# Kernel tuning notes

Hardware: AMD Instinct MI355X
Metric: run time of the kernel (lower is better)

Reference implementation:

```python
import jax, jax.numpy as jnp
import numpy as np

B, N, M, L = 16, 4096, 64, 16
NUM_FREQ, MAX_FREQ = 32, 10.0
WIDTH, NUM_MOD = 256, 512
K_GRAPH, K_INTERP = 8, 3

BANDS = 2.0 ** jnp.linspace(0.0, MAX_FREQ, NUM_FREQ)  # [32]


def setup_inputs() -> dict:
    key = jax.random.key(0)
    ks = jax.random.split(key, 12)
    return {
        "pos_g": jax.random.uniform(ks[0], (B, N, 2), dtype=jnp.float32),
        "pos_z": jax.random.uniform(ks[1], (B, M, 2), dtype=jnp.float32),
        "feat_z": jax.random.normal(ks[2], (B, M, L), dtype=jnp.float32),
        "Wl": jax.random.normal(ks[3], (L, NUM_MOD), dtype=jnp.float32) * 0.25,
        "bl": jnp.zeros((NUM_MOD,), jnp.float32),
        "Wr": jax.random.normal(ks[4], (L, NUM_MOD), dtype=jnp.float32) * 0.25,
        "W0": jax.random.normal(ks[5], (2 * 2 * NUM_FREQ, WIDTH), dtype=jnp.float32) * 0.09,
        "b0": jnp.zeros((WIDTH,), jnp.float32),
        "W1": jax.random.normal(ks[6], (WIDTH, WIDTH), dtype=jnp.float32) * 0.06,
        "b1": jnp.zeros((WIDTH,), jnp.float32),
        "W2": jax.random.normal(ks[7], (WIDTH, 1), dtype=jnp.float32) * 0.06,
        "b2": jnp.zeros((1,), jnp.float32),
    }


def _sqdist(a, b):
    # a: [B,P,2], b: [B,Q,2] -> [B,P,Q]
    return (jnp.sum(a * a, -1)[..., :, None]
            + jnp.sum(b * b, -1)[..., None, :]
            - 2.0 * jnp.einsum('bpd,bqd->bpq', a, b))


_gather = jax.vmap(lambda f, i: f[i])  # f:[M,C], i:[P,K] -> [P,K,C]


def reference(pos_g, pos_z, feat_z, Wl, bl, Wr, W0, b0, W1, b1, W2, b2):
    # --- knn_graph(z.pos, k=8, loop=False) + SAGEConv(mean aggr) ---
    d2_zz = _sqdist(pos_z, pos_z) + 1e10 * jnp.eye(M, dtype=pos_z.dtype)  # mask self-loops
    _, nbr_idx = jax.lax.top_k(-d2_zz, K_GRAPH)                 # [B,M,8]
    neigh = _gather(feat_z, nbr_idx)                            # [B,M,8,L]
    aggr = jnp.mean(neigh, axis=2)                              # [B,M,L]
    features = aggr @ Wl + bl + feat_z @ Wr                     # [B,M,512] (lin_r has no bias)

    # --- knn_interpolate(features, z.pos -> graph.pos, k=3) ---
    d2_gz = _sqdist(pos_g, pos_z)                               # [B,N,M]
    neg_d2, knn_idx = jax.lax.top_k(-d2_gz, K_INTERP)           # [B,N,3]
    w = 1.0 / jnp.maximum(-neg_d2, 1e-16)                       # inverse squared distance
    fk = _gather(features, knn_idx)                             # [B,N,3,512]
    feats_interp = jnp.sum(fk * w[..., None], axis=2) / jnp.sum(w, axis=2, keepdims=True)

    # --- positional embedding (log-sampled bands, no input concat) ---
    winded = (pos_g[:, :, None, :] * BANDS[None, None, :, None]).reshape(B, N, 2 * NUM_FREQ)
    position = jnp.concatenate([jnp.sin(winded), jnp.cos(winded)], axis=-1)  # [B,N,128]

    # --- film_translate: shift-only FiLM through hidden layers ---
    s0 = feats_interp[..., :WIDTH]
    s1 = feats_interp[..., WIDTH:]
    h = jax.nn.relu(position @ W0 + b0 + s0)                    # [B,N,256]
    h = jax.nn.relu(h @ W1 + b1 + s1)                           # [B,N,256]
    out = h @ W2 + b2                                           # [B,N,1]
    return out
```

## Files before the change

kernel.cpp:

```cpp
#include <hip/hip_runtime.h>
#include <cmath>

#define B_ 16
#define N_ 4096
#define M_ 64
#define L_ 16
#define NFREQ 32
#define NMOD 512
#define WIDTH_ 256
#define TIE_EPS 3e-7f


__global__ void __launch_bounds__(256)
feat_kernel(const float* __restrict__ pos_z, const float* __restrict__ feat_z,
            const float* __restrict__ Wl, const float* __restrict__ bl,
            const float* __restrict__ Wr, float* __restrict__ feats) {
  const int b  = blockIdx.x >> 3;
  const int cs = (blockIdx.x & 7) * 64;
  const int t  = threadIdx.x;
  __shared__ float zx[M_], zy[M_];
  __shared__ float fz[M_][L_];
  __shared__ float ag[M_][L_];
  if (t < M_) { zx[t] = pos_z[(b*M_+t)*2+0]; zy[t] = pos_z[(b*M_+t)*2+1]; }
  for (int i = t; i < M_*L_; i += 256) fz[i>>4][i&15] = feat_z[b*M_*L_ + i];
  __syncthreads();
  if (t < M_) {
    float bd[9]; int bi[9];
#pragma unroll
    for (int q=0;q<9;q++){ bd[q]=1e30f; bi[q]=0; }
    const float px = zx[t], py = zy[t];
    const float st = __fadd_rn(__fmul_rn(px,px), __fmul_rn(py,py));
    for (int j=0;j<M_;j++){
      if (j==t) continue;
      const float sj  = __fadd_rn(__fmul_rn(zx[j],zx[j]), __fmul_rn(zy[j],zy[j]));
      const float dot = __fmaf_rn(py, zy[j], __fmul_rn(px, zx[j]));
      const float d   = __fmaf_rn(-2.f, dot, __fadd_rn(st, sj));
      if (d < bd[8]) {
        int q = 8;
        while (q > 0 && bd[q-1] > d) { bd[q]=bd[q-1]; bi[q]=bi[q-1]; --q; }
        bd[q]=d; bi[q]=j;
      }
    }
    const bool hedge = (bd[8] - bd[7]) < TIE_EPS;
#pragma unroll
    for (int l=0;l<L_;l++){
      float s = 0.f;
#pragma unroll
      for (int q=0;q<7;q++) s += fz[bi[q]][l];
      s += hedge ? 0.5f*(fz[bi[7]][l] + fz[bi[8]][l]) : fz[bi[7]][l];
      ag[t][l] = s * 0.125f;
    }
  }
  __syncthreads();
  for (int idx = t; idx < M_*64; idx += 256) {
    const int i = idx >> 6, c = cs + (idx & 63);
    float a = 0.f, r = 0.f;
#pragma unroll
    for (int l=0;l<L_;l++){ a += ag[i][l]*Wl[l*NMOD+c]; r += fz[i][l]*Wr[l*NMOD+c]; }
    feats[b*M_*NMOD + i*NMOD + c] = (a + bl[c]) + r;
  }
}

__global__ void __launch_bounds__(256, 3)
fused_kernel(const float* __restrict__ pos_g, const float* __restrict__ pos_z,
             const float* __restrict__ feats,
             const float* __restrict__ W0, const float* __restrict__ b0,
             const float* __restrict__ W1, const float* __restrict__ b1,
             const float* __restrict__ W2, const float* __restrict__ b2,
             float* __restrict__ out) {
  const int b    = blockIdx.x >> 7;
  const int tile = blockIdx.x & 127;
  const int t    = threadIdx.x;
  const int g0   = tile * 32;

  __shared__ float zx[64], zy[64], gx[32], gy[32];
  __shared__ float band[NFREQ];
  __shared__ float wn[32][4];
  __shared__ int   wi[32][4];
  __shared__ float pe[32*132];
  __shared__ float h0[32*260];

  if (t < 64)      { zx[t]=pos_z[(b*64+t)*2]; zy[t]=pos_z[(b*64+t)*2+1]; }
  else if (t < 96) { const int p=t-64;
                     gx[p]=pos_g[((size_t)b*N_+g0+p)*2];
                     gy[p]=pos_g[((size_t)b*N_+g0+p)*2+1]; }
  else if (t < 96+NFREQ) { const int f=t-96;
                     const float step = __fdiv_rn(10.f, 31.f);
                     band[f] = (f==NFREQ-1) ? 1024.f
                                            : exp2f(__fmul_rn((float)f, step)); }
  __syncthreads();

  if (t < 32) {
    const float px = gx[t], py = gy[t];
    const float sg = __fadd_rn(__fmul_rn(px,px), __fmul_rn(py,py));
    float d0=1e30f,d1=1e30f,d2v=1e30f,d3=1e30f; int i0=0,i1=0,i2=0,i3=0;
    for (int j=0;j<64;j++){
      const float sz  = __fadd_rn(__fmul_rn(zx[j],zx[j]), __fmul_rn(zy[j],zy[j]));
      const float dot = __fmaf_rn(py, zy[j], __fmul_rn(px, zx[j]));
      const float d   = __fmaf_rn(-2.f, dot, __fadd_rn(sg, sz));
      if (d < d3){
        if (d < d2v){
          if (d < d1){
            if (d < d0){ d3=d2v;i3=i2; d2v=d1;i2=i1; d1=d0;i1=i0; d0=d;i0=j; }
            else       { d3=d2v;i3=i2; d2v=d1;i2=i1; d1=d;  i1=j; }
          } else       { d3=d2v;i3=i2; d2v=d;  i2=j; }
        } else         { d3=d;  i3=j; }
      }
    }
    const float wA0 = __fdiv_rn(1.f, fmaxf(d0, 1e-16f));
    const float wA1 = __fdiv_rn(1.f, fmaxf(d1, 1e-16f));
    const float wA2 = __fdiv_rn(1.f, fmaxf(d2v,1e-16f));
    const float invA = __fdiv_rn(1.f, __fadd_rn(__fadd_rn(wA0,wA1),wA2));
    if ((d3 - d2v) < TIE_EPS) {
      const float wB3 = __fdiv_rn(1.f, fmaxf(d3, 1e-16f));
      const float invB = __fdiv_rn(1.f, __fadd_rn(__fadd_rn(wA0,wA1),wB3));
      wn[t][0] = 0.5f*(wA0*invA + wA0*invB);
      wn[t][1] = 0.5f*(wA1*invA + wA1*invB);
      wn[t][2] = 0.5f*wA2*invA;
      wn[t][3] = 0.5f*wB3*invB;
    } else {
      wn[t][0] = __fmul_rn(wA0,invA);
      wn[t][1] = __fmul_rn(wA1,invA);
      wn[t][2] = __fmul_rn(wA2,invA);
      wn[t][3] = 0.f;
    }
    wi[t][0]=i0; wi[t][1]=i1; wi[t][2]=i2; wi[t][3]=i3;
  }

  for (int idx=t; idx<32*128; idx+=256){
    const int p = idx >> 7, k = idx & 127;
    const int kk = k & 63;
    const float arg = ((kk & 1) ? gy[p] : gx[p]) * band[kk>>1];
    pe[p*132+k] = (k < 64) ? sinf(arg) : cosf(arg);
  }
  __syncthreads();

  const int tp = t >> 4, tc = t & 15;
  const int p0 = tp*2;

  for (int cb=0; cb<4; ++cb){
    const int c0 = cb*64 + tc*4;
    float acc[2][4];
    {
      const float4 b4 = *reinterpret_cast<const float4*>(&b0[c0]);
      const float* bb = reinterpret_cast<const float*>(&b4);
#pragma unroll
      for (int i=0;i<2;i++){
        const int p = p0+i;
        float s[4] = {0.f,0.f,0.f,0.f};
#pragma unroll
        for (int q=0;q<4;q++){
          const float wq = wn[p][q];
          const float4 f4 = *reinterpret_cast<const float4*>(
              &feats[((size_t)(b*64 + wi[p][q]))*NMOD + c0]);
          const float* ff = reinterpret_cast<const float*>(&f4);
#pragma unroll
          for (int j=0;j<4;j++) s[j] += wq*ff[j];
        }
#pragma unroll
        for (int j=0;j<4;j++) acc[i][j] = bb[j] + s[j];
      }
    }
    float4 wb[4], pb[2];
#pragma unroll
    for (int r=0;r<4;r++) wb[r] = *reinterpret_cast<const float4*>(&W0[(size_t)r*WIDTH_ + c0]);
#pragma unroll
    for (int i=0;i<2;i++) pb[i] = *reinterpret_cast<const float4*>(&pe[(p0+i)*132]);
    for (int k=0;k<128;k+=4){
      float4 wc[4], pc[2];
#pragma unroll
      for (int r=0;r<4;r++) wc[r]=wb[r];
#pragma unroll
      for (int i=0;i<2;i++) pc[i]=pb[i];
      if (k+4 < 128){
#pragma unroll
        for (int r=0;r<4;r++) wb[r] = *reinterpret_cast<const float4*>(&W0[(size_t)(k+4+r)*WIDTH_ + c0]);
#pragma unroll
        for (int i=0;i<2;i++) pb[i] = *reinterpret_cast<const float4*>(&pe[(p0+i)*132 + k+4]);
      }
#pragma unroll
      for (int i=0;i<2;i++){
        const float* pv = reinterpret_cast<const float*>(&pc[i]);
#pragma unroll
        for (int r=0;r<4;r++){
          const float* wr = reinterpret_cast<const float*>(&wc[r]);
#pragma unroll
          for (int j=0;j<4;j++) acc[i][j] += pv[r]*wr[j];
        }
      }
    }
#pragma unroll
    for (int i=0;i<2;i++){
      float4 o; float* ov = reinterpret_cast<float*>(&o);
#pragma unroll
      for (int j=0;j<4;j++) ov[j] = fmaxf(acc[i][j], 0.f);
      *reinterpret_cast<float4*>(&h0[(p0+i)*260 + c0]) = o;
    }
  }
  __syncthreads();

  float op[2] = {0.f,0.f};
  for (int cb=0; cb<4; ++cb){
    const int c0 = cb*64 + tc*4;
    float acc[2][4];
    {
      const float4 b4 = *reinterpret_cast<const float4*>(&b1[c0]);
      const float* bb = reinterpret_cast<const float*>(&b4);
#pragma unroll
      for (int i=0;i<2;i++){
        const int p = p0+i;
        float s[4] = {0.f,0.f,0.f,0.f};
#pragma unroll
        for (int q=0;q<4;q++){
          const float wq = wn[p][q];
          const float4 f4 = *reinterpret_cast<const float4*>(
              &feats[((size_t)(b*64 + wi[p][q]))*NMOD + WIDTH_ + c0]);
          const float* ff = reinterpret_cast<const float*>(&f4);
#pragma unroll
          for (int j=0;j<4;j++) s[j] += wq*ff[j];
        }
#pragma unroll
        for (int j=0;j<4;j++) acc[i][j] = bb[j] + s[j];
      }
    }
    float4 wb[4], pb[2];
#pragma unroll
    for (int r=0;r<4;r++) wb[r] = *reinterpret_cast<const float4*>(&W1[(size_t)r*WIDTH_ + c0]);
#pragma unroll
    for (int i=0;i<2;i++) pb[i] = *reinterpret_cast<const float4*>(&h0[(p0+i)*260]);
    for (int k=0;k<256;k+=4){
      float4 wc[4], pc[2];
#pragma unroll
      for (int r=0;r<4;r++) wc[r]=wb[r];
#pragma unroll
      for (int i=0;i<2;i++) pc[i]=pb[i];
      if (k+4 < 256){
#pragma unroll
        for (int r=0;r<4;r++) wb[r] = *reinterpret_cast<const float4*>(&W1[(size_t)(k+4+r)*WIDTH_ + c0]);
#pragma unroll
        for (int i=0;i<2;i++) pb[i] = *reinterpret_cast<const float4*>(&h0[(p0+i)*260 + k+4]);
      }
#pragma unroll
      for (int i=0;i<2;i++){
        const float* pv = reinterpret_cast<const float*>(&pc[i]);
#pragma unroll
        for (int r=0;r<4;r++){
          const float* wr = reinterpret_cast<const float*>(&wc[r]);
#pragma unroll
          for (int j=0;j<4;j++) acc[i][j] += pv[r]*wr[j];
        }
      }
    }
    const float4 w24 = *reinterpret_cast<const float4*>(&W2[c0]);
    const float* w2v = reinterpret_cast<const float*>(&w24);
#pragma unroll
    for (int i=0;i<2;i++){
#pragma unroll
      for (int j=0;j<4;j++) op[i] += fmaxf(acc[i][j],0.f)*w2v[j];
    }
  }
#pragma unroll
  for (int i=0;i<2;i++){
#pragma unroll
    for (int off=1; off<16; off<<=1) op[i] += __shfl_xor(op[i], off, 64);
  }
  if (tc == 0){
    const float bb2 = b2[0];
#pragma unroll
    for (int i=0;i<2;i++) out[(size_t)b*N_ + g0 + p0 + i] = op[i] + bb2;
  }
}

extern "C" void kernel_launch(void* const* d_in, const int* in_sizes, int n_in,
                              void* d_out, int out_size, void* d_ws, size_t ws_size,
                              hipStream_t stream) {
  const float* pos_g  = (const float*)d_in[0];
  const float* pos_z  = (const float*)d_in[1];
  const float* feat_z = (const float*)d_in[2];
  const float* Wl     = (const float*)d_in[3];
  const float* bl     = (const float*)d_in[4];
  const float* Wr     = (const float*)d_in[5];
  const float* W0     = (const float*)d_in[6];
  const float* b0     = (const float*)d_in[7];
  const float* W1     = (const float*)d_in[8];
  const float* b1     = (const float*)d_in[9];
  const float* W2     = (const float*)d_in[10];
  const float* b2     = (const float*)d_in[11];
  float* feats = (float*)d_ws;

  feat_kernel<<<dim3(B_*8), dim3(256), 0, stream>>>(pos_z, feat_z, Wl, bl, Wr, feats);
  fused_kernel<<<dim3(B_*(N_/32)), dim3(256), 0, stream>>>(
      pos_g, pos_z, feats, W0, b0, W1, b1, W2, b2, (float*)d_out);
}
```

Baseline: 482.2 us.

## Split fused MLP into two register-tiled GEMM kernels with global h1 buffer

Replaces the single fused kernel with two kernels. The first builds the positional embedding and computes layer 0 with a 4x16 register-blocked outer-product GEMM, writing h1 to workspace. The second computes layer 1 plus the final projection with a shuffle reduction, and recomputes the kNN weights in each kernel. The feat kernel is also split across more blocks. The aim is better compute density and occupancy, at the cost of a 64MB h1 round trip through global memory and duplicated kNN work; the old fused path is kept as a fallback when the workspace is too small.

```diff
diff --git a/kernel.cpp b/kernel.cpp
--- a/kernel.cpp
+++ b/kernel.cpp
@@ -15,8 +15,8 @@
 feat_kernel(const float* __restrict__ pos_z, const float* __restrict__ feat_z,
             const float* __restrict__ Wl, const float* __restrict__ bl,
             const float* __restrict__ Wr, float* __restrict__ feats) {
-  const int b  = blockIdx.x >> 3;
-  const int cs = (blockIdx.x & 7) * 64;
+  const int b  = blockIdx.x >> 5;
+  const int cs = (blockIdx.x & 31) * 16;
   const int t  = threadIdx.x;
   __shared__ float zx[M_], zy[M_];
   __shared__ float fz[M_][L_];
@@ -52,8 +52,8 @@
     }
   }
   __syncthreads();
-  for (int idx = t; idx < M_*64; idx += 256) {
-    const int i = idx >> 6, c = cs + (idx & 63);
+  for (int idx = t; idx < M_*16; idx += 256) {
+    const int i = idx >> 4, c = cs + (idx & 15);
     float a = 0.f, r = 0.f;
 #pragma unroll
     for (int l=0;l<L_;l++){ a += ag[i][l]*Wl[l*NMOD+c]; r += fz[i][l]*Wr[l*NMOD+c]; }
@@ -61,36 +61,10 @@
   }
 }
 
-__global__ void __launch_bounds__(256, 3)
-fused_kernel(const float* __restrict__ pos_g, const float* __restrict__ pos_z,
-             const float* __restrict__ feats,
-             const float* __restrict__ W0, const float* __restrict__ b0,
-             const float* __restrict__ W1, const float* __restrict__ b1,
-             const float* __restrict__ W2, const float* __restrict__ b2,
-             float* __restrict__ out) {
-  const int b    = blockIdx.x >> 7;
-  const int tile = blockIdx.x & 127;
-  const int t    = threadIdx.x;
-  const int g0   = tile * 32;
-
-  __shared__ float zx[64], zy[64], gx[32], gy[32];
-  __shared__ float band[NFREQ];
-  __shared__ float wn[32][4];
-  __shared__ int   wi[32][4];
-  __shared__ float pe[32*132];
-  __shared__ float h0[32*260];
-
-  if (t < 64)      { zx[t]=pos_z[(b*64+t)*2]; zy[t]=pos_z[(b*64+t)*2+1]; }
-  else if (t < 96) { const int p=t-64;
-                     gx[p]=pos_g[((size_t)b*N_+g0+p)*2];
-                     gy[p]=pos_g[((size_t)b*N_+g0+p)*2+1]; }
-  else if (t < 96+NFREQ) { const int f=t-96;
-                     const float step = __fdiv_rn(10.f, 31.f);
-                     band[f] = (f==NFREQ-1) ? 1024.f
-                                            : exp2f(__fmul_rn((float)f, step)); }
-  __syncthreads();
-
-  if (t < 32) {
+__device__ __forceinline__ void knn3_hedge(
+    int t, const float* zx, const float* zy, const float* gx, const float* gy,
+    float (*wn)[4], int (*wi)[4]) {
+  if (t < 64) {
     const float px = gx[t], py = gy[t];
     const float sg = __fadd_rn(__fmul_rn(px,px), __fmul_rn(py,py));
     float d0=1e30f,d1=1e30f,d2v=1e30f,d3=1e30f; int i0=0,i1=0,i2=0,i3=0;
@@ -126,6 +100,302 @@
     }
     wi[t][0]=i0; wi[t][1]=i1; wi[t][2]=i2; wi[t][3]=i3;
   }
+}
+
+__global__ void __launch_bounds__(256, 4)
+b1_kernel(const float* __restrict__ pos_g, const float* __restrict__ pos_z,
+          const float* __restrict__ feats,
+          const float* __restrict__ W0, const float* __restrict__ b0,
+          float* __restrict__ h1) {
+  const int b    = blockIdx.x >> 6;
+  const int tile = blockIdx.x & 63;
+  const int t    = threadIdx.x;
+  const int g0   = tile * 64;
+
+  __shared__ float zx[64], zy[64], gx[64], gy[64];
+  __shared__ float band[NFREQ];
+  __shared__ float wn[64][4];
+  __shared__ int   wi[64][4];
+  __shared__ __align__(16) float pe_lds[64][20];
+  __shared__ __align__(16) float w_lds[16*256];
+
+  if (t < 64)       { zx[t]=pos_z[(b*64+t)*2]; zy[t]=pos_z[(b*64+t)*2+1]; }
+  else if (t < 128) { const int p=t-64;
+                      gx[p]=pos_g[((size_t)b*N_+g0+p)*2];
+                      gy[p]=pos_g[((size_t)b*N_+g0+p)*2+1]; }
+  else if (t < 128+NFREQ) { const int f=t-128;
+                      const float step = __fdiv_rn(10.f, 31.f);
+                      band[f] = (f==NFREQ-1) ? 1024.f
+                                             : exp2f(__fmul_rn((float)f, step)); }
+  __syncthreads();
+
+  knn3_hedge(t, zx, zy, gx, gy, wn, wi);
+
+  const int tp = t >> 4, tc = t & 15;
+  const int p0 = tp*4;
+
+  float acc[4][4][4];
+#pragma unroll
+  for (int i=0;i<4;i++)
+#pragma unroll
+    for (int g=0;g<4;g++)
+#pragma unroll
+      for (int j=0;j<4;j++) acc[i][g][j] = 0.f;
+
+  for (int ck = 0; ck < 8; ++ck) {
+    __syncthreads();
+    const int base = ck*16*256;
+#pragma unroll
+    for (int e = 0; e < 4; ++e) {
+      const int dw = e*1024 + t*4;
+      *reinterpret_cast<float4*>(&w_lds[dw]) =
+          *reinterpret_cast<const float4*>(&W0[base + dw]);
+    }
+#pragma unroll
+    for (int e = 0; e < 4; ++e) {
+      const int idx = t + e*256;
+      const int p = idx >> 4, kl = idx & 15;
+      const int k = ck*16 + kl;
+      const int kk = k & 63;
+      const float arg = ((kk & 1) ? gy[p] : gx[p]) * band[kk>>1];
+      pe_lds[p][kl] = (k < 64) ? sinf(arg) : cosf(arg);
+    }
+    __syncthreads();
+#pragma unroll
+    for (int ks = 0; ks < 4; ++ks) {
+      float4 pv[4];
+#pragma unroll
+      for (int i=0;i<4;i++)
+        pv[i] = *reinterpret_cast<const float4*>(&pe_lds[p0+i][ks*4]);
+#pragma unroll
+      for (int k=0;k<4;k++){
+        float4 wv[4];
+#pragma unroll
+        for (int g=0; g<4; g++)
+          wv[g] = *reinterpret_cast<const float4*>(&w_lds[(ks*4+k)*256 + g*64 + tc*4]);
+#pragma unroll
+        for (int i=0;i<4;i++){
+          const float pvk = reinterpret_cast<const float*>(&pv[i])[k];
+#pragma unroll
+          for (int g=0; g<4; g++){
+            const float* wvv = reinterpret_cast<const float*>(&wv[g]);
+#pragma unroll
+            for (int j=0;j<4;j++) acc[i][g][j] += pvk*wvv[j];
+          }
+        }
+      }
+    }
+  }
+
+  const size_t prow = (size_t)b*N_ + g0;
+#pragma unroll
+  for (int g=0; g<4; ++g){
+    const int c0 = g*64 + tc*4;
+    const float4 b4 = *reinterpret_cast<const float4*>(&b0[c0]);
+    const float* bb = reinterpret_cast<const float*>(&b4);
+#pragma unroll
+    for (int i=0;i<4;i++){
+      const int p = p0+i;
+      float s[4] = {0.f,0.f,0.f,0.f};
+#pragma unroll
+      for (int q=0;q<4;q++){
+        const float wq = wn[p][q];
+        const float4 f4 = *reinterpret_cast<const float4*>(
+            &feats[((size_t)(b*64 + wi[p][q]))*NMOD + c0]);
+        const float* ff = reinterpret_cast<const float*>(&f4);
+#pragma unroll
+        for (int j=0;j<4;j++) s[j] += wq*ff[j];
+      }
+      float4 o; float* ov = reinterpret_cast<float*>(&o);
+#pragma unroll
+      for (int j=0;j<4;j++) ov[j] = fmaxf(acc[i][g][j] + (bb[j] + s[j]), 0.f);
+      *reinterpret_cast<float4*>(&h1[(prow + p)*WIDTH_ + c0]) = o;
+    }
+  }
+}
+
+__global__ void __launch_bounds__(256, 4)
+b2_kernel(const float* __restrict__ pos_g, const float* __restrict__ pos_z,
+          const float* __restrict__ feats, const float* __restrict__ h1,
+          const float* __restrict__ W1, const float* __restrict__ b1v,
+          const float* __restrict__ W2, const float* __restrict__ b2v,
+          float* __restrict__ out) {
+  const int b    = blockIdx.x >> 6;
+  const int tile = blockIdx.x & 63;
+  const int t    = threadIdx.x;
+  const int g0   = tile * 64;
+
+  __shared__ float zx[64], zy[64], gx[64], gy[64];
+  __shared__ float wn[64][4];
+  __shared__ int   wi[64][4];
+  __shared__ __align__(16) float a_lds[64][20];
+  __shared__ __align__(16) float w_lds[16*256];
+  __shared__ float w2_lds[256];
+
+  if (t < 64)       { zx[t]=pos_z[(b*64+t)*2]; zy[t]=pos_z[(b*64+t)*2+1]; }
+  else if (t < 128) { const int p=t-64;
+                      gx[p]=pos_g[((size_t)b*N_+g0+p)*2];
+                      gy[p]=pos_g[((size_t)b*N_+g0+p)*2+1]; }
+  w2_lds[t] = W2[t];
+  __syncthreads();
+
+  knn3_hedge(t, zx, zy, gx, gy, wn, wi);
+
+  const int tp = t >> 4, tc = t & 15;
+  const int p0 = tp*4;
+  const size_t prow = (size_t)b*N_ + g0;
+
+  float acc[4][4][4];
+#pragma unroll
+  for (int i=0;i<4;i++)
+#pragma unroll
+    for (int g=0;g<4;g++)
+#pragma unroll
+      for (int j=0;j<4;j++) acc[i][g][j] = 0.f;
+
+  for (int ck = 0; ck < 16; ++ck) {
+    __syncthreads();
+    const int base = ck*16*256;
+#pragma unroll
+    for (int e = 0; e < 4; ++e) {
+      const int dw = e*1024 + t*4;
+      *reinterpret_cast<float4*>(&w_lds[dw]) =
+          *reinterpret_cast<const float4*>(&W1[base + dw]);
+    }
+    {
+      const int p = t >> 2, kq = (t & 3)*4;
+      const float4 hv = *reinterpret_cast<const float4*>(
+          &h1[(prow + p)*WIDTH_ + ck*16 + kq]);
+      *reinterpret_cast<float4*>(&a_lds[p][kq]) = hv;
+    }
+    __syncthreads();
+#pragma unroll
+    for (int ks = 0; ks < 4; ++ks) {
+      float4 pv[4];
+#pragma unroll
+      for (int i=0;i<4;i++)
+        pv[i] = *reinterpret_cast<const float4*>(&a_lds[p0+i][ks*4]);
+#pragma unroll
+      for (int k=0;k<4;k++){
+        float4 wv[4];
+#pragma unroll
+        for (int g=0; g<4; g++)
+          wv[g] = *reinterpret_cast<const float4*>(&w_lds[(ks*4+k)*256 + g*64 + tc*4]);
+#pragma unroll
+        for (int i=0;i<4;i++){
+          const float pvk = reinterpret_cast<const float*>(&pv[i])[k];
+#pragma unroll
+          for (int g=0; g<4; g++){
+            const float* wvv = reinterpret_cast<const float*>(&wv[g]);
+#pragma unroll
+            for (int j=0;j<4;j++) acc[i][g][j] += pvk*wvv[j];
+          }
+        }
+      }
+    }
+  }
+
+  float op[4] = {0.f,0.f,0.f,0.f};
+#pragma unroll
+  for (int g=0; g<4; ++g){
+    const int c0 = g*64 + tc*4;
+    const float4 b4 = *reinterpret_cast<const float4*>(&b1v[c0]);
+    const float* bb = reinterpret_cast<const float*>(&b4);
+#pragma unroll
+    for (int i=0;i<4;i++){
+      const int p = p0+i;
+      float s[4] = {0.f,0.f,0.f,0.f};
+#pragma unroll
+      for (int q=0;q<4;q++){
+        const float wq = wn[p][q];
+        const float4 f4 = *reinterpret_cast<const float4*>(
+            &feats[((size_t)(b*64 + wi[p][q]))*NMOD + WIDTH_ + c0]);
+        const float* ff = reinterpret_cast<const float*>(&f4);
+#pragma unroll
+        for (int j=0;j<4;j++) s[j] += wq*ff[j];
+      }
+#pragma unroll
+      for (int j=0;j<4;j++)
+        op[i] += fmaxf(acc[i][g][j] + (bb[j] + s[j]), 0.f) * w2_lds[c0+j];
+    }
+  }
+#pragma unroll
+  for (int i=0;i<4;i++){
+#pragma unroll
+    for (int off=1; off<16; off<<=1) op[i] += __shfl_xor(op[i], off, 64);
+  }
+  if (tc == 0){
+    const float bb2 = b2v[0];
+#pragma unroll
+    for (int i=0;i<4;i++) out[prow + p0 + i] = op[i] + bb2;
+  }
+}
+
+__global__ void __launch_bounds__(256, 3)
+fused_kernel(const float* __restrict__ pos_g, const float* __restrict__ pos_z,
+             const float* __restrict__ feats,
+             const float* __restrict__ W0, const float* __restrict__ b0,
+             const float* __restrict__ W1, const float* __restrict__ b1,
+             const float* __restrict__ W2, const float* __restrict__ b2,
+             float* __restrict__ out) {
+  const int b    = blockIdx.x >> 7;
+  const int tile = blockIdx.x & 127;
+  const int t    = threadIdx.x;
+  const int g0   = tile * 32;
+
+  __shared__ float zx[64], zy[64], gx[32], gy[32];
+  __shared__ float band[NFREQ];
+  __shared__ float wn[32][4];
+  __shared__ int   wi[32][4];
+  __shared__ float pe[32*132];
+  __shared__ float h0[32*260];
+
+  if (t < 64)      { zx[t]=pos_z[(b*64+t)*2]; zy[t]=pos_z[(b*64+t)*2+1]; }
+  else if (t < 96) { const int p=t-64;
+                     gx[p]=pos_g[((size_t)b*N_+g0+p)*2];
+                     gy[p]=pos_g[((size_t)b*N_+g0+p)*2+1]; }
+  else if (t < 96+NFREQ) { const int f=t-96;
+                     const float step = __fdiv_rn(10.f, 31.f);
+                     band[f] = (f==NFREQ-1) ? 1024.f
+                                            : exp2f(__fmul_rn((float)f, step)); }
+  __syncthreads();
+
+  if (t < 32) {
+    const float px = gx[t], py = gy[t];
+    const float sg = __fadd_rn(__fmul_rn(px,px), __fmul_rn(py,py));
+    float d0=1e30f,d1=1e30f,d2v=1e30f,d3=1e30f; int i0=0,i1=0,i2=0,i3=0;
+    for (int j=0;j<64;j++){
+      const float sz  = __fadd_rn(__fmul_rn(zx[j],zx[j]), __fmul_rn(zy[j],zy[j]));
+      const float dot = __fmaf_rn(py, zy[j], __fmul_rn(px, zx[j]));
+      const float d   = __fmaf_rn(-2.f, dot, __fadd_rn(sg, sz));
+      if (d < d3){
+        if (d < d2v){
+          if (d < d1){
+            if (d < d0){ d3=d2v;i3=i2; d2v=d1;i2=i1; d1=d0;i1=i0; d0=d;i0=j; }
+            else       { d3=d2v;i3=i2; d2v=d1;i2=i1; d1=d;  i1=j; }
+          } else       { d3=d2v;i3=i2; d2v=d;  i2=j; }
+        } else         { d3=d;  i3=j; }
+      }
+    }
+    const float wA0 = __fdiv_rn(1.f, fmaxf(d0, 1e-16f));
+    const float wA1 = __fdiv_rn(1.f, fmaxf(d1, 1e-16f));
+    const float wA2 = __fdiv_rn(1.f, fmaxf(d2v,1e-16f));
+    const float invA = __fdiv_rn(1.f, __fadd_rn(__fadd_rn(wA0,wA1),wA2));
+    if ((d3 - d2v) < TIE_EPS) {
+      const float wB3 = __fdiv_rn(1.f, fmaxf(d3, 1e-16f));
+      const float invB = __fdiv_rn(1.f, __fadd_rn(__fadd_rn(wA0,wA1),wB3));
+      wn[t][0] = 0.5f*(wA0*invA + wA0*invB);
+      wn[t][1] = 0.5f*(wA1*invA + wA1*invB);
+      wn[t][2] = 0.5f*wA2*invA;
+      wn[t][3] = 0.5f*wB3*invB;
+    } else {
+      wn[t][0] = __fmul_rn(wA0,invA);
+      wn[t][1] = __fmul_rn(wA1,invA);
+      wn[t][2] = __fmul_rn(wA2,invA);
+      wn[t][3] = 0.f;
+    }
+    wi[t][0]=i0; wi[t][1]=i1; wi[t][2]=i2; wi[t][3]=i3;
+  }
 
   for (int idx=t; idx<32*128; idx+=256){
     const int p = idx >> 7, k = idx & 127;
@@ -286,9 +556,21 @@
   const float* b1     = (const float*)d_in[9];
   const float* W2     = (const float*)d_in[10];
   const float* b2     = (const float*)d_in[11];
+
+  const size_t FEATS_BYTES = (size_t)B_ * M_ * NMOD * sizeof(float);
+  const size_t H1_BYTES    = (size_t)B_ * N_ * WIDTH_ * sizeof(float);
   float* feats = (float*)d_ws;
 
-  feat_kernel<<<dim3(B_*8), dim3(256), 0, stream>>>(pos_z, feat_z, Wl, bl, Wr, feats);
-  fused_kernel<<<dim3(B_*(N_/32)), dim3(256), 0, stream>>>(
-      pos_g, pos_z, feats, W0, b0, W1, b1, W2, b2, (float*)d_out);
+  feat_kernel<<<dim3(B_*32), dim3(256), 0, stream>>>(pos_z, feat_z, Wl, bl, Wr, feats);
+
+  if (ws_size >= FEATS_BYTES + H1_BYTES) {
+    float* h1 = (float*)((char*)d_ws + FEATS_BYTES);
+    b1_kernel<<<dim3(B_*(N_/64)), dim3(256), 0, stream>>>(
+        pos_g, pos_z, feats, W0, b0, h1);
+    b2_kernel<<<dim3(B_*(N_/64)), dim3(256), 0, stream>>>(
+        pos_g, pos_z, feats, h1, W1, b1, W2, b2, (float*)d_out);
+  } else {
+    fused_kernel<<<dim3(B_*(N_/32)), dim3(256), 0, stream>>>(
+        pos_g, pos_z, feats, W0, b0, W1, b1, W2, b2, (float*)d_out);
+  }
 }
```

Result: faster. 433.1 us (-10.2%).
